# Kernel tuning notes

Hardware: AMD Instinct MI355X
Metric: run time of the kernel (lower is better)

## Reference

```python
import jax, jax.numpy as jnp
import numpy as np
from jax import lax

C = 256
EPS = 1e-5
DN = ('NCHW', 'OIHW', 'NCHW')


def dw_conv(x, w, dilation):
    # depthwise conv, groups=C, stride 1, 'same' padding for odd kernels
    K = w.shape[2]
    pad = dilation * (K - 1) // 2
    return lax.conv_general_dilated(
        x, w, window_strides=(1, 1), padding=[(pad, pad), (pad, pad)],
        rhs_dilation=(dilation, dilation), dimension_numbers=DN,
        feature_group_count=C)


def batchnorm(y, gamma, beta):
    # training-mode BN: batch stats over (N,H,W), biased variance (torch semantics)
    m = jnp.mean(y, axis=(0, 2, 3), keepdims=True)
    v = jnp.mean((y - m) ** 2, axis=(0, 2, 3), keepdims=True)
    g = gamma.reshape(1, C, 1, 1)
    b = beta.reshape(1, C, 1, 1)
    return (y - m) * (g * lax.rsqrt(v + EPS)) + b


def setup_inputs() -> dict:
    key = jax.random.key(0)
    ks = jax.random.split(key, 20)
    d = {
        'x': jax.random.normal(ks[0], (8, C, 112, 112), jnp.float32),
        'w_origin': jax.random.normal(ks[1], (C, 1, 11, 11), jnp.float32) * 0.05,
        'g_origin': jax.random.uniform(ks[2], (C,), jnp.float32, 0.5, 1.5),
        'b_origin': jax.random.normal(ks[3], (C,), jnp.float32) * 0.05,
    }
    branches = [('k5_1', 5), ('k7_1', 7), ('k5_2', 5), ('k3_3', 3), ('k3_5', 3)]
    i = 4
    for name, K in branches:
        d[f'w_{name}'] = jax.random.normal(ks[i], (C, 1, K, K), jnp.float32) * 0.05
        d[f'g_{name}'] = jax.random.uniform(ks[i + 1], (C,), jnp.float32, 0.5, 1.5)
        d[f'b_{name}'] = jax.random.normal(ks[i + 2], (C,), jnp.float32) * 0.05
        i += 3
    return d


def reference(x, w_origin, g_origin, b_origin,
              w_k5_1, g_k5_1, b_k5_1,
              w_k7_1, g_k7_1, b_k7_1,
              w_k5_2, g_k5_2, b_k5_2,
              w_k3_3, g_k3_3, b_k3_3,
              w_k3_5, g_k3_5, b_k3_5):
    out = batchnorm(dw_conv(x, w_origin, 1), g_origin, b_origin)
    branches = [
        (w_k5_1, g_k5_1, b_k5_1, 1),
        (w_k7_1, g_k7_1, b_k7_1, 1),
        (w_k5_2, g_k5_2, b_k5_2, 2),
        (w_k3_3, g_k3_3, b_k3_3, 3),
        (w_k3_5, g_k3_5, b_k3_5, 5),
    ]
    for w, g, b, r in branches:
        out = out + batchnorm(dw_conv(x, w, r), g, b)
    return out
```

## Files before the change

kernel.cpp:

```cpp
#include <hip/hip_runtime.h>
#include <math.h>

#define NCH   256
#define HH    112
#define WW    112
#define NB    8
#define PLANE (HH*WW)
#define LSTR  132
#define LOFF  9
#define COLG  (WW/8)
#define NTASK (HH*COLG)
#define BNEPS 1e-5f

template<int K, int DIL>
__device__ __forceinline__ void branch_row(float acc[8], const float* __restrict__ wc,
                                           const int dy, const float xr[18]) {
  constexpr int P = (K - 1) / 2;
  if (dy % DIL != 0) return;
  const int q = dy / DIL;
  if (q < -P || q > P) return;
  const float* wrow = wc + (q + P) * K;
  #pragma unroll
  for (int kj = 0; kj < K; ++kj) {
    const float wv = wrow[kj];
    const int off = 5 + (kj - P) * DIL;
    #pragma unroll
    for (int j = 0; j < 8; ++j)
      acc[j] = fmaf(wv, xr[j + off], acc[j]);
  }
}

__device__ __forceinline__ void load_plane_to_lds(float* tile, const float* __restrict__ x,
                                                  int plane, int tid) {
  float4* t4 = reinterpret_cast<float4*>(tile);
  #pragma unroll 4
  for (int i = tid; i < HH * LSTR / 4; i += 256) t4[i] = make_float4(0.f, 0.f, 0.f, 0.f);
  __syncthreads();
  const float4* xp4 = reinterpret_cast<const float4*>(x + (size_t)plane * PLANE);
  for (int i = tid; i < PLANE / 4; i += 256) {
    const int r  = i / (WW / 4);
    const int c4 = (i - r * (WW / 4)) * 4;
    const float4 v = xp4[i];
    float* d = &tile[r * LSTR + LOFF + c4];
    d[0] = v.x; d[1] = v.y; d[2] = v.z; d[3] = v.w;
  }
  __syncthreads();
}

extern "C" __global__ void __launch_bounds__(256)
k_stats(const float* __restrict__ x,
        const float* __restrict__ w0, const float* __restrict__ w1,
        const float* __restrict__ w2, const float* __restrict__ w3,
        const float* __restrict__ w4, const float* __restrict__ w5,
        float* __restrict__ partials)
{
  __shared__ float tile[HH * LSTR];
  const int plane = blockIdx.x;
  const int ch    = plane & (NCH - 1);
  const int tid   = threadIdx.x;

  load_plane_to_lds(tile, x, plane, tid);

  const float* wc0 = w0 + ch * 121;
  const float* wc1 = w1 + ch * 25;
  const float* wc2 = w2 + ch * 49;
  const float* wc3 = w3 + ch * 25;
  const float* wc4 = w4 + ch * 9;
  const float* wc5 = w5 + ch * 9;

  float s[6]  = {0.f, 0.f, 0.f, 0.f, 0.f, 0.f};
  float ss[6] = {0.f, 0.f, 0.f, 0.f, 0.f, 0.f};

  for (int t = tid; t < NTASK; t += 256) {
    const int r  = t / COLG;
    const int c0 = (t - r * COLG) * 8;
    float acc[6][8];
    #pragma unroll
    for (int b = 0; b < 6; ++b) {
      #pragma unroll
      for (int j = 0; j < 8; ++j) acc[b][j] = 0.f;
    }
    #pragma unroll
    for (int dy = -5; dy <= 5; ++dy) {
      const int rr = r + dy;
      float xr[18];
      if (rr >= 0 && rr < HH) {
        const float* lrow = &tile[rr * LSTR + c0 + LOFF - 5];
        #pragma unroll
        for (int k = 0; k < 18; ++k) xr[k] = lrow[k];
      } else {
        #pragma unroll
        for (int k = 0; k < 18; ++k) xr[k] = 0.f;
      }
      branch_row<11, 1>(acc[0], wc0, dy, xr);
      branch_row< 5, 1>(acc[1], wc1, dy, xr);
      branch_row< 7, 1>(acc[2], wc2, dy, xr);
      branch_row< 5, 2>(acc[3], wc3, dy, xr);
      branch_row< 3, 3>(acc[4], wc4, dy, xr);
      branch_row< 3, 5>(acc[5], wc5, dy, xr);
    }
    #pragma unroll
    for (int b = 0; b < 6; ++b) {
      #pragma unroll
      for (int j = 0; j < 8; ++j) { const float v = acc[b][j]; s[b] += v; ss[b] += v * v; }
    }
  }

  __syncthreads();
  #pragma unroll
  for (int b = 0; b < 6; ++b) {
    #pragma unroll
    for (int off = 32; off > 0; off >>= 1) {
      s[b]  += __shfl_xor(s[b],  off, 64);
      ss[b] += __shfl_xor(ss[b], off, 64);
    }
  }
  const int lane = tid & 63, wid = tid >> 6;
  if (lane == 0) {
    #pragma unroll
    for (int b = 0; b < 6; ++b) { tile[wid * 12 + 2 * b] = s[b]; tile[wid * 12 + 2 * b + 1] = ss[b]; }
  }
  __syncthreads();
  if (tid < 12) {
    partials[(size_t)plane * 12 + tid] =
        tile[tid] + tile[12 + tid] + tile[24 + tid] + tile[36 + tid];
  }
}

template<int K, int DIL>
__device__ __forceinline__ void merge_k(float* wmv, const float* __restrict__ wc, const float sc) {
  constexpr int P = (K - 1) / 2;
  #pragma unroll
  for (int ki = 0; ki < K; ++ki) {
    #pragma unroll
    for (int kj = 0; kj < K; ++kj) {
      const int idx = ((ki - P) * DIL + 5) * 11 + ((kj - P) * DIL + 5);
      wmv[idx] += sc * wc[ki * K + kj];
    }
  }
}

extern "C" __global__ void __launch_bounds__(256)
k_merge(const float* __restrict__ partials,
        const float* __restrict__ w0, const float* __restrict__ g0, const float* __restrict__ b0,
        const float* __restrict__ w1, const float* __restrict__ g1, const float* __restrict__ b1,
        const float* __restrict__ w2, const float* __restrict__ g2, const float* __restrict__ b2,
        const float* __restrict__ w3, const float* __restrict__ g3, const float* __restrict__ b3,
        const float* __restrict__ w4, const float* __restrict__ g4, const float* __restrict__ b4,
        const float* __restrict__ w5, const float* __restrict__ g5, const float* __restrict__ b5,
        float* __restrict__ wm, float* __restrict__ bias)
{
  const int ch = threadIdx.x;
  const float invc = 1.f / (float)(NB * PLANE);
  float wmv[121];
  #pragma unroll
  for (int i = 0; i < 121; ++i) wmv[i] = 0.f;
  float bacc = 0.f;

#define BR_STATS(B)                                                                 \
    float S = 0.f, SS = 0.f;                                                        \
    for (int n = 0; n < NB; ++n) {                                                  \
      const float* p = &partials[(size_t)(n * NCH + ch) * 12 + 2 * (B)];            \
      S += p[0]; SS += p[1];                                                        \
    }                                                                               \
    const float m = S * invc;                                                       \
    const float v = fmaxf(SS * invc - m * m, 0.f);

  { BR_STATS(0) const float sc = g0[ch] / sqrtf(v + BNEPS); bacc += b0[ch] - m * sc; merge_k<11, 1>(wmv, w0 + ch * 121, sc); }
  { BR_STATS(1) const float sc = g1[ch] / sqrtf(v + BNEPS); bacc += b1[ch] - m * sc; merge_k< 5, 1>(wmv, w1 + ch * 25,  sc); }
  { BR_STATS(2) const float sc = g2[ch] / sqrtf(v + BNEPS); bacc += b2[ch] - m * sc; merge_k< 7, 1>(wmv, w2 + ch * 49,  sc); }
  { BR_STATS(3) const float sc = g3[ch] / sqrtf(v + BNEPS); bacc += b3[ch] - m * sc; merge_k< 5, 2>(wmv, w3 + ch * 25,  sc); }
  { BR_STATS(4) const float sc = g4[ch] / sqrtf(v + BNEPS); bacc += b4[ch] - m * sc; merge_k< 3, 3>(wmv, w4 + ch * 9,   sc); }
  { BR_STATS(5) const float sc = g5[ch] / sqrtf(v + BNEPS); bacc += b5[ch] - m * sc; merge_k< 3, 5>(wmv, w5 + ch * 9,   sc); }
#undef BR_STATS

  #pragma unroll
  for (int i = 0; i < 121; ++i) wm[(size_t)ch * 121 + i] = wmv[i];
  bias[ch] = bacc;
}

extern "C" __global__ void __launch_bounds__(256)
k_conv(const float* __restrict__ x, const float* __restrict__ wm,
       const float* __restrict__ bias, float* __restrict__ out)
{
  __shared__ float tile[HH * LSTR];
  const int plane = blockIdx.x;
  const int ch    = plane & (NCH - 1);
  const int tid   = threadIdx.x;

  load_plane_to_lds(tile, x, plane, tid);

  const float* wmc = wm + (size_t)ch * 121;
  const float bc   = bias[ch];
  float* op = out + (size_t)plane * PLANE;

  for (int t = tid; t < NTASK; t += 256) {
    const int r  = t / COLG;
    const int c0 = (t - r * COLG) * 8;
    float acc[8];
    #pragma unroll
    for (int j = 0; j < 8; ++j) acc[j] = bc;

    #pragma unroll
    for (int dy = -5; dy <= 5; ++dy) {
      const int rr = r + dy;
      float xr[18];
      if (rr >= 0 && rr < HH) {
        const float* lrow = &tile[rr * LSTR + c0 + LOFF - 5];
        #pragma unroll
        for (int k = 0; k < 18; ++k) xr[k] = lrow[k];
      } else {
        #pragma unroll
        for (int k = 0; k < 18; ++k) xr[k] = 0.f;
      }
      const float* wrow = wmc + (dy + 5) * 11;
      #pragma unroll
      for (int kj = 0; kj < 11; ++kj) {
        const float wv = wrow[kj];
        #pragma unroll
        for (int j = 0; j < 8; ++j) acc[j] = fmaf(wv, xr[j + kj], acc[j]);
      }
    }
    float4 o0 = make_float4(acc[0], acc[1], acc[2], acc[3]);
    float4 o1 = make_float4(acc[4], acc[5], acc[6], acc[7]);
    float* dst = &op[r * WW + c0];
    reinterpret_cast<float4*>(dst)[0] = o0;
    reinterpret_cast<float4*>(dst)[1] = o1;
  }
}

extern "C" void kernel_launch(void* const* d_in, const int* in_sizes, int n_in,
                              void* d_out, int out_size, void* d_ws, size_t ws_size,
                              hipStream_t stream) {
  (void)in_sizes; (void)n_in; (void)out_size; (void)ws_size;
  const float* x   = (const float*)d_in[0];
  const float* w0  = (const float*)d_in[1];
  const float* g0  = (const float*)d_in[2];
  const float* b0  = (const float*)d_in[3];
  const float* w1  = (const float*)d_in[4];
  const float* g1  = (const float*)d_in[5];
  const float* b1  = (const float*)d_in[6];
  const float* w2  = (const float*)d_in[7];
  const float* g2  = (const float*)d_in[8];
  const float* b2  = (const float*)d_in[9];
  const float* w3  = (const float*)d_in[10];
  const float* g3  = (const float*)d_in[11];
  const float* b3  = (const float*)d_in[12];
  const float* w4  = (const float*)d_in[13];
  const float* g4  = (const float*)d_in[14];
  const float* b4  = (const float*)d_in[15];
  const float* w5  = (const float*)d_in[16];
  const float* g5  = (const float*)d_in[17];
  const float* b5  = (const float*)d_in[18];

  float* partials = (float*)d_ws;
  float* wm       = partials + 2048 * 12;
  float* bias     = wm + 256 * 121;
  float* outp     = (float*)d_out;

  k_stats<<<dim3(NB * NCH), dim3(256), 0, stream>>>(x, w0, w1, w2, w3, w4, w5, partials);
  k_merge<<<dim3(1), dim3(256), 0, stream>>>(partials,
      w0, g0, b0, w1, g1, b1, w2, g2, b2, w3, g3, b3, w4, g4, b4, w5, g5, b5,
      wm, bias);
  k_conv<<<dim3(NB * NCH), dim3(256), 0, stream>>>(x, wm, bias, outp);
}
```

Measured before the change: 456.8 us.

## Split each plane into two row halves with smaller LDS tiles and vectorized row reads

Each plane is now handled by two blocks, each loading a 66-row halo tile instead of the full 112-row plane. The smaller LDS footprint lets more blocks fit per CU, backed by launch_bounds(256,4), and doubles the grid size. Row reads from LDS become five float4 loads with no branch, relying on zeroed halo rows instead of per-row bounds checks. In exchange, the halo rows are loaded twice, the merge step reads twice as many partial sums, and the stats kernel switches to a column-major task mapping.

```diff
diff --git a/kernel.cpp b/kernel.cpp
--- a/kernel.cpp
+++ b/kernel.cpp
@@ -9,12 +9,14 @@
 #define LSTR  132
 #define LOFF  9
 #define COLG  (WW/8)
-#define NTASK (HH*COLG)
+#define ROWS_PER 56
+#define TROWS 66
+#define NTASK (ROWS_PER*COLG)
 #define BNEPS 1e-5f
 
 template<int K, int DIL>
 __device__ __forceinline__ void branch_row(float acc[8], const float* __restrict__ wc,
-                                           const int dy, const float xr[18]) {
+                                           const int dy, const float xr[20]) {
   constexpr int P = (K - 1) / 2;
   if (dy % DIL != 0) return;
   const int q = dy / DIL;
@@ -30,36 +32,50 @@
   }
 }
 
-__device__ __forceinline__ void load_plane_to_lds(float* tile, const float* __restrict__ x,
-                                                  int plane, int tid) {
+__device__ __forceinline__ void load_half_to_lds(float* tile, const float* __restrict__ x,
+                                                 int plane, int r0, int tid) {
   float4* t4 = reinterpret_cast<float4*>(tile);
-  #pragma unroll 4
-  for (int i = tid; i < HH * LSTR / 4; i += 256) t4[i] = make_float4(0.f, 0.f, 0.f, 0.f);
-  __syncthreads();
-  const float4* xp4 = reinterpret_cast<const float4*>(x + (size_t)plane * PLANE);
-  for (int i = tid; i < PLANE / 4; i += 256) {
-    const int r  = i / (WW / 4);
-    const int c4 = (i - r * (WW / 4)) * 4;
-    const float4 v = xp4[i];
-    float* d = &tile[r * LSTR + LOFF + c4];
-    d[0] = v.x; d[1] = v.y; d[2] = v.z; d[3] = v.w;
-  }
-  __syncthreads();
-}
-
-extern "C" __global__ void __launch_bounds__(256)
+  #pragma unroll 2
+  for (int i = tid; i < TROWS * LSTR / 4; i += 256) t4[i] = make_float4(0.f, 0.f, 0.f, 0.f);
+  __syncthreads();
+  const float* xp = x + (size_t)plane * PLANE;
+  for (int i = tid; i < TROWS * (WW / 4); i += 256) {
+    const int tr = i / (WW / 4);
+    const int c4 = (i - tr * (WW / 4)) * 4;
+    const int ir = r0 - 5 + tr;
+    if (ir >= 0 && ir < HH) {
+      const float4 v = *reinterpret_cast<const float4*>(xp + ir * WW + c4);
+      float* d = &tile[tr * LSTR + LOFF + c4];
+      d[0] = v.x; d[1] = v.y; d[2] = v.z; d[3] = v.w;
+    }
+  }
+  __syncthreads();
+}
+
+__device__ __forceinline__ void read_row20(float xr[20], const float* base) {
+  const float4* lp = reinterpret_cast<const float4*>(base);
+  #pragma unroll
+  for (int q = 0; q < 5; ++q) {
+    const float4 v = lp[q];
+    xr[4 * q] = v.x; xr[4 * q + 1] = v.y; xr[4 * q + 2] = v.z; xr[4 * q + 3] = v.w;
+  }
+}
+
+extern "C" __global__ void __launch_bounds__(256, 4)
 k_stats(const float* __restrict__ x,
         const float* __restrict__ w0, const float* __restrict__ w1,
         const float* __restrict__ w2, const float* __restrict__ w3,
         const float* __restrict__ w4, const float* __restrict__ w5,
         float* __restrict__ partials)
 {
-  __shared__ float tile[HH * LSTR];
-  const int plane = blockIdx.x;
+  __shared__ __align__(16) float tile[TROWS * LSTR];
+  const int bid   = blockIdx.x;
+  const int plane = bid >> 1;
+  const int r0    = (bid & 1) * ROWS_PER;
   const int ch    = plane & (NCH - 1);
   const int tid   = threadIdx.x;
 
-  load_plane_to_lds(tile, x, plane, tid);
+  load_half_to_lds(tile, x, plane, r0, tid);
 
   const float* wc0 = w0 + ch * 121;
   const float* wc1 = w1 + ch * 25;
@@ -72,8 +88,9 @@
   float ss[6] = {0.f, 0.f, 0.f, 0.f, 0.f, 0.f};
 
   for (int t = tid; t < NTASK; t += 256) {
-    const int r  = t / COLG;
-    const int c0 = (t - r * COLG) * 8;
+    const int rl = t % ROWS_PER;
+    const int c0 = (t / ROWS_PER) * 8;
+    const float* base = &tile[(rl + 5) * LSTR + c0 + 4];
     float acc[6][8];
     #pragma unroll
     for (int b = 0; b < 6; ++b) {
@@ -82,16 +99,8 @@
     }
     #pragma unroll
     for (int dy = -5; dy <= 5; ++dy) {
-      const int rr = r + dy;
-      float xr[18];
-      if (rr >= 0 && rr < HH) {
-        const float* lrow = &tile[rr * LSTR + c0 + LOFF - 5];
-        #pragma unroll
-        for (int k = 0; k < 18; ++k) xr[k] = lrow[k];
-      } else {
-        #pragma unroll
-        for (int k = 0; k < 18; ++k) xr[k] = 0.f;
-      }
+      float xr[20];
+      read_row20(xr, base + dy * LSTR);
       branch_row<11, 1>(acc[0], wc0, dy, xr);
       branch_row< 5, 1>(acc[1], wc1, dy, xr);
       branch_row< 7, 1>(acc[2], wc2, dy, xr);
@@ -122,7 +131,7 @@
   }
   __syncthreads();
   if (tid < 12) {
-    partials[(size_t)plane * 12 + tid] =
+    partials[(size_t)bid * 12 + tid] =
         tile[tid] + tile[12 + tid] + tile[24 + tid] + tile[36 + tid];
   }
 }
@@ -160,8 +169,10 @@
 #define BR_STATS(B)                                                                 \
     float S = 0.f, SS = 0.f;                                                        \
     for (int n = 0; n < NB; ++n) {                                                  \
-      const float* p = &partials[(size_t)(n * NCH + ch) * 12 + 2 * (B)];            \
-      S += p[0]; SS += p[1];                                                        \
+      for (int h = 0; h < 2; ++h) {                                                 \
+        const float* p = &partials[(size_t)((n * NCH + ch) * 2 + h) * 12 + 2 * (B)];\
+        S += p[0]; SS += p[1];                                                      \
+      }                                                                             \
     }                                                                               \
     const float m = S * invc;                                                       \
     const float v = fmaxf(SS * invc - m * m, 0.f);
@@ -179,40 +190,35 @@
   bias[ch] = bacc;
 }
 
-extern "C" __global__ void __launch_bounds__(256)
+extern "C" __global__ void __launch_bounds__(256, 4)
 k_conv(const float* __restrict__ x, const float* __restrict__ wm,
        const float* __restrict__ bias, float* __restrict__ out)
 {
-  __shared__ float tile[HH * LSTR];
-  const int plane = blockIdx.x;
+  __shared__ __align__(16) float tile[TROWS * LSTR];
+  const int bid   = blockIdx.x;
+  const int plane = bid >> 1;
+  const int r0    = (bid & 1) * ROWS_PER;
   const int ch    = plane & (NCH - 1);
   const int tid   = threadIdx.x;
 
-  load_plane_to_lds(tile, x, plane, tid);
+  load_half_to_lds(tile, x, plane, r0, tid);
 
   const float* wmc = wm + (size_t)ch * 121;
   const float bc   = bias[ch];
   float* op = out + (size_t)plane * PLANE;
 
   for (int t = tid; t < NTASK; t += 256) {
-    const int r  = t / COLG;
-    const int c0 = (t - r * COLG) * 8;
+    const int rl = t / COLG;
+    const int c0 = (t - rl * COLG) * 8;
+    const float* base = &tile[(rl + 5) * LSTR + c0 + 4];
     float acc[8];
     #pragma unroll
     for (int j = 0; j < 8; ++j) acc[j] = bc;
 
     #pragma unroll
     for (int dy = -5; dy <= 5; ++dy) {
-      const int rr = r + dy;
-      float xr[18];
-      if (rr >= 0 && rr < HH) {
-        const float* lrow = &tile[rr * LSTR + c0 + LOFF - 5];
-        #pragma unroll
-        for (int k = 0; k < 18; ++k) xr[k] = lrow[k];
-      } else {
-        #pragma unroll
-        for (int k = 0; k < 18; ++k) xr[k] = 0.f;
-      }
+      float xr[20];
+      read_row20(xr, base + dy * LSTR);
       const float* wrow = wmc + (dy + 5) * 11;
       #pragma unroll
       for (int kj = 0; kj < 11; ++kj) {
@@ -223,7 +229,7 @@
     }
     float4 o0 = make_float4(acc[0], acc[1], acc[2], acc[3]);
     float4 o1 = make_float4(acc[4], acc[5], acc[6], acc[7]);
-    float* dst = &op[r * WW + c0];
+    float* dst = &op[(r0 + rl) * WW + c0];
     reinterpret_cast<float4*>(dst)[0] = o0;
     reinterpret_cast<float4*>(dst)[1] = o1;
   }
@@ -254,13 +260,13 @@
   const float* b5  = (const float*)d_in[18];
 
   float* partials = (float*)d_ws;
-  float* wm       = partials + 2048 * 12;
+  float* wm       = partials + 4096 * 12;
   float* bias     = wm + 256 * 121;
   float* outp     = (float*)d_out;
 
-  k_stats<<<dim3(NB * NCH), dim3(256), 0, stream>>>(x, w0, w1, w2, w3, w4, w5, partials);
+  k_stats<<<dim3(NB * NCH * 2), dim3(256), 0, stream>>>(x, w0, w1, w2, w3, w4, w5, partials);
   k_merge<<<dim3(1), dim3(256), 0, stream>>>(partials,
       w0, g0, b0, w1, g1, b1, w2, g2, b2, w3, g3, b3, w4, g4, b4, w5, g5, b5,
       wm, bias);
-  k_conv<<<dim3(NB * NCH), dim3(256), 0, stream>>>(x, wm, bias, outp);
-}
+  k_conv<<<dim3(NB * NCH * 2), dim3(256), 0, stream>>>(x, wm, bias, outp);
+}
```

After: 446.2 us. -2.3%, faster.
